# Kernel tuning notes

Hardware: AMD Instinct MI355X
Metric: run time of the kernel (lower is better)

## Reference

```python
import jax, jax.numpy as jnp
import numpy as np

POS_SCALE = 50.0
LEN_SCALE = 500.0

N_NODES = 100000
N_EDGES = 600000
IN_DIM = 128
HID_DIM = 128


def setup_inputs() -> dict:
    key = jax.random.key(0)
    ks = jax.random.split(key, 12)
    x = jax.random.normal(ks[0], (N_NODES, IN_DIM), dtype=jnp.float32)
    positions = jax.random.randint(ks[1], (N_NODES,), 0, 50, dtype=jnp.int64)
    lengths = jax.random.randint(ks[2], (N_NODES,), 0, 500, dtype=jnp.int64)
    edge_index = jax.random.randint(ks[3], (2, N_EDGES), 0, N_NODES, dtype=jnp.int64)
    reranker_scores = jax.random.normal(ks[4], (N_NODES,), dtype=jnp.float32)
    s = 1.0 / np.sqrt(IN_DIM + 2)
    fp_w = jax.random.uniform(ks[5], (IN_DIM + 2, IN_DIM), minval=-s, maxval=s, dtype=jnp.float32)
    fp_b = jnp.zeros((IN_DIM,), jnp.float32)
    s2 = 1.0 / np.sqrt(IN_DIM)
    lin_l_w = jax.random.uniform(ks[6], (IN_DIM, HID_DIM), minval=-s2, maxval=s2, dtype=jnp.float32)
    lin_l_b = jnp.zeros((HID_DIM,), jnp.float32)
    lin_r_w = jax.random.uniform(ks[7], (IN_DIM, HID_DIM), minval=-s2, maxval=s2, dtype=jnp.float32)
    res_w = jax.random.uniform(ks[8], (IN_DIM, HID_DIM), minval=-s2, maxval=s2, dtype=jnp.float32)
    res_b = jnp.zeros((HID_DIM,), jnp.float32)
    s3 = 1.0 / np.sqrt(HID_DIM)
    sh_w = jax.random.uniform(ks[9], (HID_DIM, 1), minval=-s3, maxval=s3, dtype=jnp.float32)
    sh_b = jnp.zeros((1,), jnp.float32)
    alpha = jnp.asarray(0.65, jnp.float32)
    return {
        "x": x, "positions": positions, "lengths": lengths,
        "edge_index": edge_index, "reranker_scores": reranker_scores,
        "fp_w": fp_w, "fp_b": fp_b,
        "lin_l_w": lin_l_w, "lin_l_b": lin_l_b, "lin_r_w": lin_r_w,
        "res_w": res_w, "res_b": res_b,
        "sh_w": sh_w, "sh_b": sh_b, "alpha": alpha,
    }


def reference(x, positions, lengths, edge_index, reranker_scores,
              fp_w, fp_b, lin_l_w, lin_l_b, lin_r_w, res_w, res_b,
              sh_w, sh_b, alpha):
    n = x.shape[0]
    # position/length features
    pos_feat = positions[:, None].astype(x.dtype) / POS_SCALE
    len_feat = lengths[:, None].astype(x.dtype) / LEN_SCALE
    xf = jnp.concatenate([x, pos_feat, len_feat], axis=-1)  # [N, D+2]
    xf = xf @ fp_w + fp_b                                   # [N, D]
    h_in = xf @ res_w + res_b                               # residual proj [N, H]
    # SAGEConv with mean aggregation: out = lin_l(mean_{j->i} x_j) + lin_r(x_i)
    src, dst = edge_index[0], edge_index[1]
    msg_sum = jax.ops.segment_sum(xf[src], dst, num_segments=n)          # [N, D]
    cnt = jax.ops.segment_sum(jnp.ones((src.shape[0], 1), xf.dtype), dst, num_segments=n)
    agg = msg_sum / jnp.maximum(cnt, 1.0)
    h = jax.nn.relu(agg @ lin_l_w + lin_l_b + xf @ lin_r_w)  # [N, H]
    # dropout is identity in eval mode
    h = h + h_in
    gnn_scores = (h @ sh_w + sh_b)[:, 0]                     # [N]
    a = jax.nn.sigmoid(alpha)
    return a * reranker_scores + (1.0 - a) * gnn_scores
```

## Files before the change

### kernel.cpp

```cpp
#include <hip/hip_runtime.h>
#include <hip/hip_bf16.h>
#include <cstdint>

#define D 128
#define LDSPITCH 136
#define CAP 32

typedef __attribute__((ext_vector_type(4))) float f32x4;
typedef __attribute__((ext_vector_type(8))) short s16x8;

__device__ __forceinline__ unsigned short f2b(float f) {
    union { float f; uint32_t u; } v; v.f = f;
    uint32_t b = v.u + 0x7fffu + ((v.u >> 16) & 1u);
    return (unsigned short)(b >> 16);
}
__device__ __forceinline__ float b2f(unsigned short u) {
    union { uint32_t u; float f; } v; v.u = ((uint32_t)u) << 16; return v.f;
}

__global__ __launch_bounds__(256) void k_prep(
    const float* __restrict__ fp_w, const float* __restrict__ lin_l_w,
    const float* __restrict__ lin_r_w,
    unsigned short* __restrict__ Btf, unsigned short* __restrict__ Btl,
    unsigned short* __restrict__ Btr,
    const float* __restrict__ res_w, const float* __restrict__ res_b,
    const float* __restrict__ sh_w, const float* __restrict__ sh_b,
    const float* __restrict__ alpha, float* __restrict__ c1, float* __restrict__ scal,
    int* __restrict__ cursor, int N) {
    int bid = blockIdx.x, tid = threadIdx.x;
    if (bid < 192) {
        int m = bid >> 6;
        int i = (bid & 63) * 256 + tid;
        const float* src = (m == 0) ? fp_w : (m == 1) ? lin_l_w : lin_r_w;
        unsigned short* dst = (m == 0) ? Btf : (m == 1) ? Btl : Btr;
        int k = i >> 7, n = i & 127;
        dst[n * D + k] = f2b(src[k * D + n]);
    } else if (bid == 192) {
        if (tid < 128) {
            float s = 0.f;
            for (int j = 0; j < D; ++j) s += res_w[tid * D + j] * sh_w[j];
            c1[tid] = s;
            if (tid == 0) {
                float c0 = 0.f;
                for (int j = 0; j < D; ++j) c0 += res_b[j] * sh_w[j];
                c0 += sh_b[0];
                float a = 1.f / (1.f + expf(-alpha[0]));
                scal[0] = a; scal[1] = c0;
            }
        }
    } else {
        int i = ((bid - 193) * 256 + tid) * 4;
        if (i < N) {
            if (i + 3 < N) *(int4*)(cursor + i) = (int4){0, 0, 0, 0};
            else { for (int k = i; k < N; ++k) cursor[k] = 0; }
        }
    }
}

__global__ __launch_bounds__(256) void k_gemm1(
    const float* __restrict__ x, unsigned short* __restrict__ xb,
    const int* __restrict__ positions, const int* __restrict__ lengths,
    const unsigned short* __restrict__ Btf,
    const float* __restrict__ fp_w, const float* __restrict__ fp_b,
    const float* __restrict__ c1, float* __restrict__ d1, int N, int mb,
    const int* __restrict__ ei, int* __restrict__ cursor, int* __restrict__ srcs, int E) {
    if (blockIdx.x >= mb) {
        int e = (blockIdx.x - mb) * 256 + threadIdx.x;
        if (e < E) {
            int src = ei[e];
            int dst = ei[E + e];
            int pos = atomicAdd(&cursor[dst], 1);
            if (pos < CAP) srcs[dst * CAP + pos] = src;
        }
        return;
    }
    int lane = threadIdx.x & 63;
    int wv = threadIdx.x >> 6;
    int col = lane & 15, q = lane >> 4;
    int row0 = blockIdx.x * 64 + wv * 16;
    int arow = row0 + col; if (arow > N - 1) arow = N - 1;

    f32x4 acc[8];
#pragma unroll
    for (int nt = 0; nt < 8; ++nt) acc[nt] = (f32x4){0.f, 0.f, 0.f, 0.f};

#pragma unroll
    for (int ks = 0; ks < 4; ++ks) {
        const float* xp = x + (size_t)arow * D + ks * 32 + q * 8;
        float4 a0 = *(const float4*)xp;
        float4 a1 = *(const float4*)(xp + 4);
        s16x8 af;
        af[0] = (short)f2b(a0.x); af[1] = (short)f2b(a0.y);
        af[2] = (short)f2b(a0.z); af[3] = (short)f2b(a0.w);
        af[4] = (short)f2b(a1.x); af[5] = (short)f2b(a1.y);
        af[6] = (short)f2b(a1.z); af[7] = (short)f2b(a1.w);
#pragma unroll
        for (int nt = 0; nt < 8; ++nt) {
            s16x8 bf = *(const s16x8*)(Btf + (size_t)(nt * 16 + col) * D + ks * 32 + q * 8);
            acc[nt] = __builtin_amdgcn_mfma_f32_16x16x32_bf16(af, bf, acc[nt], 0, 0, 0);
        }
    }

    float pf[4], lf[4];
#pragma unroll
    for (int r = 0; r < 4; ++r) {
        int rr = row0 + q * 4 + r; int rc = rr < N ? rr : N - 1;
        pf[r] = (float)positions[rc] * (1.0f / 50.0f);
        lf[r] = (float)lengths[rc] * (1.0f / 500.0f);
    }
    float sdot[4] = {0.f, 0.f, 0.f, 0.f};
#pragma unroll
    for (int nt = 0; nt < 8; ++nt) {
        int n = nt * 16 + col;
        float bias = fp_b[n];
        float w128 = fp_w[128 * D + n];
        float w129 = fp_w[129 * D + n];
        float c1v = c1[n];
#pragma unroll
        for (int r = 0; r < 4; ++r) {
            float t = acc[nt][r] + bias + pf[r] * w128 + lf[r] * w129;
            int rr = row0 + q * 4 + r;
            if (rr < N) xb[(size_t)rr * D + n] = f2b(t);
            sdot[r] += t * c1v;
        }
    }
#pragma unroll
    for (int r = 0; r < 4; ++r) {
        float s = sdot[r];
        s += __shfl_xor(s, 1, 64);
        s += __shfl_xor(s, 2, 64);
        s += __shfl_xor(s, 4, 64);
        s += __shfl_xor(s, 8, 64);
        if (col == 0) {
            int rr = row0 + q * 4 + r;
            if (rr < N) d1[rr] = s;
        }
    }
}

__global__ __launch_bounds__(256) void k_gemm2(
    const unsigned short* __restrict__ xfb,
    const int* __restrict__ cursor, const int* __restrict__ srcs,
    const unsigned short* __restrict__ Btl, const unsigned short* __restrict__ Btr,
    const float* __restrict__ lin_l_b, const float* __restrict__ sh_w,
    const float* __restrict__ rer, const float* __restrict__ d1,
    const float* __restrict__ scal, float* __restrict__ out, int N) {
    __shared__ unsigned short agg[64 * LDSPITCH];
    int lane = threadIdx.x & 63;
    int wv = threadIdx.x >> 6;
    int li = lane & 15, q = lane >> 4;
    int wrow0 = blockIdx.x * 64 + wv * 16;

#pragma unroll
    for (int rr = 0; rr < 4; ++rr) {
        int row = wrow0 + rr * 4 + q;
        float t[8] = {0.f, 0.f, 0.f, 0.f, 0.f, 0.f, 0.f, 0.f};
        int deg = 0;
        if (row < N) {
            deg = cursor[row]; if (deg > CAP) deg = CAP;
            const int* sp = srcs + (size_t)row * CAP;
            int dm1 = deg - 1;
            for (int j = 0; j < deg; j += 8) {
                int4 ia = *(const int4*)(sp + (j     < dm1 ? j     : (dm1 & ~3)));
                int4 ib;
                {
                    int jb = j + 4 <= dm1 ? j + 4 : (dm1 & ~3);
                    ib = *(const int4*)(sp + jb);
                }
                int idx[8];
                idx[0] = sp[j];
                idx[1] = j + 1 <= dm1 ? ia.y : sp[dm1];
                idx[2] = j + 2 <= dm1 ? ia.z : sp[dm1];
                idx[3] = j + 3 <= dm1 ? ia.w : sp[dm1];
                idx[4] = j + 4 <= dm1 ? ib.x : sp[dm1];
                idx[5] = j + 5 <= dm1 ? ib.y : sp[dm1];
                idx[6] = j + 6 <= dm1 ? ib.z : sp[dm1];
                idx[7] = j + 7 <= dm1 ? ib.w : sp[dm1];
                s16x8 v[8];
#pragma unroll
                for (int k = 0; k < 8; ++k)
                    v[k] = *(const s16x8*)(xfb + (size_t)idx[k] * D + li * 8);
                float w[8];
#pragma unroll
                for (int k = 0; k < 8; ++k) w[k] = (j + k < deg) ? 1.f : 0.f;
#pragma unroll
                for (int k = 0; k < 8; ++k)
#pragma unroll
                    for (int k2 = 0; k2 < 8; ++k2)
                        t[k2] += w[k] * b2f((unsigned short)v[k][k2]);
            }
        }
        float rc = 1.0f / (float)(deg > 0 ? deg : 1);
        s16x8 o;
#pragma unroll
        for (int k2 = 0; k2 < 8; ++k2) o[k2] = (short)f2b(t[k2] * rc);
        *(s16x8*)(agg + (wv * 16 + rr * 4 + q) * LDSPITCH + li * 8) = o;
    }

    int arow = wrow0 + li; if (arow > N - 1) arow = N - 1;

    f32x4 acc[8];
#pragma unroll
    for (int nt = 0; nt < 8; ++nt) acc[nt] = (f32x4){0.f, 0.f, 0.f, 0.f};

#pragma unroll
    for (int ks = 0; ks < 4; ++ks) {
        s16x8 af = *(const s16x8*)(agg + (wv * 16 + li) * LDSPITCH + ks * 32 + q * 8);
#pragma unroll
        for (int nt = 0; nt < 8; ++nt) {
            s16x8 bf = *(const s16x8*)(Btl + (size_t)(nt * 16 + li) * D + ks * 32 + q * 8);
            acc[nt] = __builtin_amdgcn_mfma_f32_16x16x32_bf16(af, bf, acc[nt], 0, 0, 0);
        }
    }
#pragma unroll
    for (int ks = 0; ks < 4; ++ks) {
        s16x8 af = *(const s16x8*)(xfb + (size_t)arow * D + ks * 32 + q * 8);
#pragma unroll
        for (int nt = 0; nt < 8; ++nt) {
            s16x8 bf = *(const s16x8*)(Btr + (size_t)(nt * 16 + li) * D + ks * 32 + q * 8);
            acc[nt] = __builtin_amdgcn_mfma_f32_16x16x32_bf16(af, bf, acc[nt], 0, 0, 0);
        }
    }

    float a = scal[0], c0 = scal[1];
    float sdot[4] = {0.f, 0.f, 0.f, 0.f};
#pragma unroll
    for (int nt = 0; nt < 8; ++nt) {
        int n = nt * 16 + li;
        float bias = lin_l_b[n];
        float shw = sh_w[n];
#pragma unroll
        for (int r = 0; r < 4; ++r) {
            float t = acc[nt][r] + bias;
            sdot[r] += fmaxf(t, 0.f) * shw;
        }
    }
#pragma unroll
    for (int r = 0; r < 4; ++r) {
        float s = sdot[r];
        s += __shfl_xor(s, 1, 64);
        s += __shfl_xor(s, 2, 64);
        s += __shfl_xor(s, 4, 64);
        s += __shfl_xor(s, 8, 64);
        if (li == 0) {
            int rr = wrow0 + q * 4 + r;
            if (rr < N) out[rr] = a * rer[rr] + (1.f - a) * (c0 + d1[rr] + s);
        }
    }
}

extern "C" void kernel_launch(void* const* d_in, const int* in_sizes, int n_in,
                              void* d_out, int out_size, void* d_ws, size_t ws_size,
                              hipStream_t stream) {
    const float* x        = (const float*)d_in[0];
    const int*   positions= (const int*)d_in[1];
    const int*   lengths  = (const int*)d_in[2];
    const int*   ei       = (const int*)d_in[3];
    const float* rer      = (const float*)d_in[4];
    const float* fp_w     = (const float*)d_in[5];
    const float* fp_b     = (const float*)d_in[6];
    const float* lin_l_w  = (const float*)d_in[7];
    const float* lin_l_b  = (const float*)d_in[8];
    const float* lin_r_w  = (const float*)d_in[9];
    const float* res_w    = (const float*)d_in[10];
    const float* res_b    = (const float*)d_in[11];
    const float* sh_w     = (const float*)d_in[12];
    const float* sh_b     = (const float*)d_in[13];
    const float* alpha    = (const float*)d_in[14];
    int N = in_sizes[1];
    int E = in_sizes[3] / 2;
    float* out = (float*)d_out;

    char* ws = (char*)d_ws;
    size_t off = 0;
    auto alloc = [&](size_t bytes) -> void* {
        void* p = ws + off;
        off = (off + bytes + 255) & ~(size_t)255;
        return p;
    };
    unsigned short* xb  = (unsigned short*)alloc((size_t)N * D * 2);
    int* srcs    = (int*)alloc((size_t)N * CAP * 4);
    int* cursor  = (int*)alloc((size_t)N * 4);
    float* d1    = (float*)alloc((size_t)N * 4);
    unsigned short* Btf = (unsigned short*)alloc(D * D * 2);
    unsigned short* Btl = (unsigned short*)alloc(D * D * 2);
    unsigned short* Btr = (unsigned short*)alloc(D * D * 2);
    float* c1    = (float*)alloc(D * 4);
    float* scal  = (float*)alloc(16);

    int mb = (N + 63) / 64;
    int cb = (E + 255) / 256;
    int zb = (N + 1023) / 1024;

    k_prep<<<193 + zb, 256, 0, stream>>>(fp_w, lin_l_w, lin_r_w, Btf, Btl, Btr,
                                         res_w, res_b, sh_w, sh_b, alpha, c1, scal,
                                         cursor, N);
    k_gemm1<<<mb + cb, 256, 0, stream>>>(x, xb, positions, lengths, Btf, fp_w, fp_b,
                                         c1, d1, N, mb, ei, cursor, srcs, E);
    k_gemm2<<<mb, 256, 0, stream>>>(xb, cursor, srcs, Btl, Btr, lin_l_b, sh_w, rer, d1, scal, out, N);
}
```

Baseline: 250.7 us.

## Pad neighbor lists with zero sentinel row and interleave gathers across rows

```diff
diff --git a/kernel.cpp b/kernel.cpp
--- a/kernel.cpp
+++ b/kernel.cpp
@@ -26,7 +26,8 @@
     const float* __restrict__ res_w, const float* __restrict__ res_b,
     const float* __restrict__ sh_w, const float* __restrict__ sh_b,
     const float* __restrict__ alpha, float* __restrict__ c1, float* __restrict__ scal,
-    int* __restrict__ cursor, int N) {
+    int* __restrict__ cursor, int* __restrict__ srcs, unsigned short* __restrict__ xb,
+    int N, int zb) {
     int bid = blockIdx.x, tid = threadIdx.x;
     if (bid < 192) {
         int m = bid >> 6;
@@ -47,13 +48,18 @@
                 float a = 1.f / (1.f + expf(-alpha[0]));
                 scal[0] = a; scal[1] = c0;
             }
-        }
-    } else {
+        } else if (tid < 192) {
+            ((unsigned int*)(xb + (size_t)N * D))[tid - 128] = 0u;
+        }
+    } else if (bid < 193 + zb) {
         int i = ((bid - 193) * 256 + tid) * 4;
         if (i < N) {
             if (i + 3 < N) *(int4*)(cursor + i) = (int4){0, 0, 0, 0};
             else { for (int k = i; k < N; ++k) cursor[k] = 0; }
         }
+    } else {
+        int i = ((bid - 193 - zb) * 256 + tid) * 4;
+        if (i < N * CAP) *(int4*)(srcs + i) = (int4){N, N, N, N};
     }
 }
 
@@ -151,49 +157,63 @@
     int li = lane & 15, q = lane >> 4;
     int wrow0 = blockIdx.x * 64 + wv * 16;
 
+    int degs[4];
+    const int* sp[4];
 #pragma unroll
     for (int rr = 0; rr < 4; ++rr) {
         int row = wrow0 + rr * 4 + q;
-        float t[8] = {0.f, 0.f, 0.f, 0.f, 0.f, 0.f, 0.f, 0.f};
-        int deg = 0;
-        if (row < N) {
-            deg = cursor[row]; if (deg > CAP) deg = CAP;
-            const int* sp = srcs + (size_t)row * CAP;
-            int dm1 = deg - 1;
-            for (int j = 0; j < deg; j += 8) {
-                int4 ia = *(const int4*)(sp + (j     < dm1 ? j     : (dm1 & ~3)));
-                int4 ib;
-                {
-                    int jb = j + 4 <= dm1 ? j + 4 : (dm1 & ~3);
-                    ib = *(const int4*)(sp + jb);
-                }
-                int idx[8];
-                idx[0] = sp[j];
-                idx[1] = j + 1 <= dm1 ? ia.y : sp[dm1];
-                idx[2] = j + 2 <= dm1 ? ia.z : sp[dm1];
-                idx[3] = j + 3 <= dm1 ? ia.w : sp[dm1];
-                idx[4] = j + 4 <= dm1 ? ib.x : sp[dm1];
-                idx[5] = j + 5 <= dm1 ? ib.y : sp[dm1];
-                idx[6] = j + 6 <= dm1 ? ib.z : sp[dm1];
-                idx[7] = j + 7 <= dm1 ? ib.w : sp[dm1];
-                s16x8 v[8];
-#pragma unroll
-                for (int k = 0; k < 8; ++k)
-                    v[k] = *(const s16x8*)(xfb + (size_t)idx[k] * D + li * 8);
-                float w[8];
-#pragma unroll
-                for (int k = 0; k < 8; ++k) w[k] = (j + k < deg) ? 1.f : 0.f;
-#pragma unroll
-                for (int k = 0; k < 8; ++k)
-#pragma unroll
-                    for (int k2 = 0; k2 < 8; ++k2)
-                        t[k2] += w[k] * b2f((unsigned short)v[k][k2]);
+        int ok = row < N;
+        int dg = ok ? cursor[row] : 0;
+        degs[rr] = dg > CAP ? CAP : dg;
+        sp[rr] = srcs + (size_t)(ok ? row : 0) * CAP;
+    }
+    int dmax = degs[0] > degs[1] ? degs[0] : degs[1];
+    if (degs[2] > dmax) dmax = degs[2];
+    if (degs[3] > dmax) dmax = degs[3];
+    dmax = max(dmax, __shfl_xor(dmax, 16, 64));
+    dmax = max(dmax, __shfl_xor(dmax, 32, 64));
+    int rounds = (dmax + 7) >> 3;
+
+    float t[4][8];
+#pragma unroll
+    for (int rr = 0; rr < 4; ++rr)
+#pragma unroll
+        for (int k2 = 0; k2 < 8; ++k2) t[rr][k2] = 0.f;
+
+    for (int jr = 0; jr < rounds; ++jr) {
+        int j = jr * 8;
+#pragma unroll
+        for (int rr = 0; rr < 4; ++rr) {
+            int4 ia = *(const int4*)(sp[rr] + j);
+            int4 ib = *(const int4*)(sp[rr] + j + 4);
+            s16x8 v0 = *(const s16x8*)(xfb + (size_t)ia.x * D + li * 8);
+            s16x8 v1 = *(const s16x8*)(xfb + (size_t)ia.y * D + li * 8);
+            s16x8 v2 = *(const s16x8*)(xfb + (size_t)ia.z * D + li * 8);
+            s16x8 v3 = *(const s16x8*)(xfb + (size_t)ia.w * D + li * 8);
+            s16x8 v4 = *(const s16x8*)(xfb + (size_t)ib.x * D + li * 8);
+            s16x8 v5 = *(const s16x8*)(xfb + (size_t)ib.y * D + li * 8);
+            s16x8 v6 = *(const s16x8*)(xfb + (size_t)ib.z * D + li * 8);
+            s16x8 v7 = *(const s16x8*)(xfb + (size_t)ib.w * D + li * 8);
+#pragma unroll
+            for (int k2 = 0; k2 < 8; ++k2) {
+                t[rr][k2] += b2f((unsigned short)v0[k2]);
+                t[rr][k2] += b2f((unsigned short)v1[k2]);
+                t[rr][k2] += b2f((unsigned short)v2[k2]);
+                t[rr][k2] += b2f((unsigned short)v3[k2]);
+                t[rr][k2] += b2f((unsigned short)v4[k2]);
+                t[rr][k2] += b2f((unsigned short)v5[k2]);
+                t[rr][k2] += b2f((unsigned short)v6[k2]);
+                t[rr][k2] += b2f((unsigned short)v7[k2]);
             }
         }
-        float rc = 1.0f / (float)(deg > 0 ? deg : 1);
+    }
+
+#pragma unroll
+    for (int rr = 0; rr < 4; ++rr) {
+        float rc = 1.0f / (float)(degs[rr] > 0 ? degs[rr] : 1);
         s16x8 o;
 #pragma unroll
-        for (int k2 = 0; k2 < 8; ++k2) o[k2] = (short)f2b(t[k2] * rc);
+        for (int k2 = 0; k2 < 8; ++k2) o[k2] = (short)f2b(t[rr][k2] * rc);
         *(s16x8*)(agg + (wv * 16 + rr * 4 + q) * LDSPITCH + li * 8) = o;
     }
 
@@ -231,8 +251,8 @@
         float shw = sh_w[n];
 #pragma unroll
         for (int r = 0; r < 4; ++r) {
-            float t = acc[nt][r] + bias;
-            sdot[r] += fmaxf(t, 0.f) * shw;
+            float t2 = acc[nt][r] + bias;
+            sdot[r] += fmaxf(t2, 0.f) * shw;
         }
     }
 #pragma unroll
@@ -278,7 +298,7 @@
         off = (off + bytes + 255) & ~(size_t)255;
         return p;
     };
-    unsigned short* xb  = (unsigned short*)alloc((size_t)N * D * 2);
+    unsigned short* xb  = (unsigned short*)alloc((size_t)(N + 1) * D * 2);
     int* srcs    = (int*)alloc((size_t)N * CAP * 4);
     int* cursor  = (int*)alloc((size_t)N * 4);
     float* d1    = (float*)alloc((size_t)N * 4);
@@ -291,10 +311,11 @@
     int mb = (N + 63) / 64;
     int cb = (E + 255) / 256;
     int zb = (N + 1023) / 1024;
-
-    k_prep<<<193 + zb, 256, 0, stream>>>(fp_w, lin_l_w, lin_r_w, Btf, Btl, Btr,
-                                         res_w, res_b, sh_w, sh_b, alpha, c1, scal,
-                                         cursor, N);
+    int sb = (N * CAP / 4 + 255) / 256;
+
+    k_prep<<<193 + zb + sb, 256, 0, stream>>>(fp_w, lin_l_w, lin_r_w, Btf, Btl, Btr,
+                                              res_w, res_b, sh_w, sh_b, alpha, c1, scal,
+                                              cursor, srcs, xb, N, zb);
     k_gemm1<<<mb + cb, 256, 0, stream>>>(x, xb, positions, lengths, Btf, fp_w, fp_b,
                                          c1, d1, N, mb, ei, cursor, srcs, E);
     k_gemm2<<<mb, 256, 0, stream>>>(xb, cursor, srcs, Btl, Btr, lin_l_b, sh_w, rer, d1, scal, out, N);
```

New measurement: 260.1 us. 1.04x slower.
